# Performance work log

Hardware: AMD Instinct MI355X
Metric: run time of the kernel (lower is better)

## Reference

```python
import jax, jax.numpy as jnp
import numpy as np

D = 768
H = 12
HD = D // H
NQ = 100
KV = 257
SEQ = NQ + KV
BS = 32


def layer_norm(x, g, b):
    # torch LayerNorm computed in fp32 then cast back (LayerNorm subclass)
    xf = x.astype(jnp.float32)
    m = xf.mean(-1, keepdims=True)
    v = ((xf - m) ** 2).mean(-1, keepdims=True)
    return ((xf - m) / jnp.sqrt(v + 1e-5) * g + b).astype(x.dtype)


def setup_inputs() -> dict:
    key = jax.random.key(0)
    ks = jax.random.split(key, 8)
    s = 0.02
    return {
        "y": jax.random.normal(ks[0], (SEQ, BS, D), jnp.float32),
        "attn_mask": jax.random.bernoulli(ks[1], 0.3, (BS, NQ, KV)),
        "in_proj_w": jax.random.normal(ks[2], (3 * D, D), jnp.float32) * s,
        "in_proj_b": jnp.zeros((3 * D,), jnp.float32),
        "new_q_w": jax.random.normal(ks[3], (D, D), jnp.float32) * s,
        "new_q_b": jnp.zeros((D,), jnp.float32),
        "out_w": jax.random.normal(ks[4], (D, D), jnp.float32) * s,
        "out_b": jnp.zeros((D,), jnp.float32),
        "ln1_g": jnp.ones((D,), jnp.float32),
        "ln1_b": jnp.zeros((D,), jnp.float32),
        "ln2_g": jnp.ones((D,), jnp.float32),
        "ln2_b": jnp.zeros((D,), jnp.float32),
        "fc_w": jax.random.normal(ks[5], (4 * D, D), jnp.float32) * s,
        "fc_b": jnp.zeros((4 * D,), jnp.float32),
        "proj_w": jax.random.normal(ks[6], (D, 4 * D), jnp.float32) * s,
        "proj_b": jnp.zeros((D,), jnp.float32),
    }


def _attention(x, attn_mask, in_proj_w, in_proj_b, new_q_w, new_q_b, out_w, out_b):
    # x: [seq, bs, D] (already ln_1'd); attn_mask: [bs, nq, kv] bool
    seq, bs, d = x.shape
    nq = attn_mask.shape[1]
    scale = 1.0 / np.sqrt(HD)
    # k/v (and the clip queries) come from the detached non-query tokens
    xkv = jax.lax.stop_gradient(x[nq:])  # [kv, bs, D]
    qkv = xkv @ in_proj_w.T + in_proj_b
    q, k, v = jnp.split(qkv, 3, axis=-1)

    def heads(t):  # [S, bs, D] -> [bs, H, S, hd]
        return t.reshape(t.shape[0], bs, H, HD).transpose(1, 2, 0, 3)

    q = heads(q) * scale
    k = heads(k)
    v = heads(v)
    # regular (clip) attention over shared k/v
    clip_attn = jnp.einsum('bhld,bhmd->bhlm', q, k)
    clip_out = jnp.einsum('bhlm,bhmd->bhld', jax.nn.softmax(clip_attn, axis=-1), v)
    # mask-conditioned queries via new_q_proj (NOT detached)
    new_q = heads(x[:nq] @ new_q_w.T + new_q_b) * scale  # [bs, H, nq, hd]
    bias = jnp.where(attn_mask[:, None], -jnp.inf, 0.0).astype(q.dtype)  # [bs,1,nq,kv]
    mask_attn = jnp.einsum('bhqd,bhmd->bhqm', new_q, k) + bias
    mask_out = jnp.einsum('bhqm,bhmd->bhqd', jax.nn.softmax(mask_attn, axis=-1), v)

    def merge(t):  # [bs, H, S, hd] -> [S, bs, D]
        return t.transpose(2, 0, 1, 3).reshape(t.shape[2], bs, d)

    attn_out = jnp.concatenate([merge(mask_out), merge(clip_out)], axis=0)
    return attn_out @ out_w.T + out_b


def reference(y, attn_mask, in_proj_w, in_proj_b, new_q_w, new_q_b, out_w, out_b,
              ln1_g, ln1_b, ln2_g, ln2_b, fc_w, fc_b, proj_w, proj_b):
    x = layer_norm(y, ln1_g, ln1_b)
    y = y + _attention(x, attn_mask, in_proj_w, in_proj_b, new_q_w, new_q_b, out_w, out_b)
    h = layer_norm(y, ln2_g, ln2_b)
    h = h @ fc_w.T + fc_b
    h = h * jax.nn.sigmoid(1.702 * h)  # QuickGELU
    return y + (h @ proj_w.T + proj_b)
```

## Files before the change

### kernel.cpp

```cpp
#include <hip/hip_runtime.h>


typedef short bf16x8 __attribute__((ext_vector_type(8)));
typedef float f32x4 __attribute__((ext_vector_type(4)));
typedef unsigned short u16;
typedef unsigned long long u64;

__device__ __forceinline__ u16 f2b(float f) {
    unsigned u = __builtin_bit_cast(unsigned, f);
    u = (u + 0x7fffu + ((u >> 16) & 1u)) >> 16;
    return (u16)u;
}
__device__ __forceinline__ float b2f(u16 h) {
    unsigned u = ((unsigned)h) << 16;
    return __builtin_bit_cast(float, u);
}
__device__ __forceinline__ unsigned pack2(float a, float b) {
    return (unsigned)f2b(a) | ((unsigned)f2b(b) << 16);
}
__device__ __forceinline__ void g2l16(const void* g, void* l) {
    __builtin_amdgcn_global_load_lds(
        (__attribute__((address_space(1))) void*)g,
        (__attribute__((address_space(3))) void*)l, 16, 0, 0);
}

__global__ __launch_bounds__(256) void cvt5_kernel(
    const float* __restrict__ s0, const float* __restrict__ s1, const float* __restrict__ s2,
    const float* __restrict__ s3, const float* __restrict__ s4, u16* __restrict__ dst)
{
    int i = blockIdx.x * 256 + threadIdx.x;
    int stride = gridDim.x * 256;
    for (; i < 1916928; i += stride) {
        const float* src; int off;
        if (i < 442368)       { src = s0; off = i; }
        else if (i < 589824)  { src = s1; off = i - 442368; }
        else if (i < 737280)  { src = s2; off = i - 589824; }
        else if (i < 1327104) { src = s3; off = i - 737280; }
        else                  { src = s4; off = i - 1327104; }
        float4 v = ((const float4*)src)[off];
        ushort4 o;
        o.x = f2b(v.x); o.y = f2b(v.y); o.z = f2b(v.z); o.w = f2b(v.w);
        ((ushort4*)dst)[i] = o;
    }
}

__global__ __launch_bounds__(256) void mask_pack(const int* __restrict__ m, u64* __restrict__ o) {
    int row = blockIdx.x * 4 + (threadIdx.x >> 6);
    int lane = threadIdx.x & 63;
    if (row >= 3200) return;
    const int* r = m + (size_t)row * 257;
    u64 w0 = __ballot(r[lane] != 0);
    u64 w1 = __ballot(r[64 + lane] != 0);
    u64 w2 = __ballot(r[128 + lane] != 0);
    u64 w3 = __ballot(r[192 + lane] != 0);
    u64 w4 = __ballot(lane == 0 && r[256] != 0);
    if (lane == 0) {
        u64* p = o + (size_t)row * 5;
        p[0] = w0; p[1] = w1; p[2] = w2; p[3] = w3; p[4] = w4;
    }
}

__global__ __launch_bounds__(256) void ln_kernel(
    const float* __restrict__ in, const float* __restrict__ g, const float* __restrict__ be,
    u16* __restrict__ out, int nrows)
{
    int row = blockIdx.x * 4 + (threadIdx.x >> 6);
    int lane = threadIdx.x & 63;
    if (row >= nrows) return;
    const float* p = in + (size_t)row * 768;
    float4 a0 = *(const float4*)(p + lane * 4);
    float4 a1 = *(const float4*)(p + 256 + lane * 4);
    float4 a2 = *(const float4*)(p + 512 + lane * 4);
    float s = a0.x + a0.y + a0.z + a0.w + a1.x + a1.y + a1.z + a1.w + a2.x + a2.y + a2.z + a2.w;
    for (int o = 32; o; o >>= 1) s += __shfl_xor(s, o);
    float mean = s * (1.f / 768.f);
    float vs = 0.f;
#define SQA(t) { float dx; dx = t.x-mean; vs += dx*dx; dx = t.y-mean; vs += dx*dx; dx = t.z-mean; vs += dx*dx; dx = t.w-mean; vs += dx*dx; }
    SQA(a0) SQA(a1) SQA(a2)
#undef SQA
    for (int o = 32; o; o >>= 1) vs += __shfl_xor(vs, o);
    float rstd = rsqrtf(vs * (1.f / 768.f) + 1e-5f);
    u16* orow = out + (size_t)row * 768;
#pragma unroll
    for (int i = 0; i < 3; ++i) {
        int d = i * 256 + lane * 4;
        float4 av = (i == 0) ? a0 : ((i == 1) ? a1 : a2);
        float4 gv = *(const float4*)(g + d);
        float4 bv = *(const float4*)(be + d);
        ushort4 ov;
        ov.x = f2b((av.x - mean) * rstd * gv.x + bv.x);
        ov.y = f2b((av.y - mean) * rstd * gv.y + bv.y);
        ov.z = f2b((av.z - mean) * rstd * gv.z + bv.z);
        ov.w = f2b((av.w - mean) * rstd * gv.w + bv.w);
        *(ushort4*)(orow + d) = ov;
    }
}

template<int ACT, int OUTBF, int RES>
__global__ __launch_bounds__(256) void gemm_bt(
    const u16* __restrict__ A, const u16* __restrict__ B,
    const float* __restrict__ bias, const float* __restrict__ res,
    void* __restrict__ Cp, int M, int N, int K)
{
    __shared__ u16 Al[2][128 * 32];
    __shared__ u16 Bl[2][128 * 32];
    const int t = threadIdx.x;
    const int lane = t & 63, w = t >> 6;
    const int wr = w >> 1, wc = w & 1;
    const int m0 = blockIdx.x * 128, n0 = blockIdx.y * 128;
    const int fr = lane & 15, fg = lane >> 4;

    const int srow = lane >> 2;
    const int scol = (lane & 3) * 8;
    int ar0 = m0 + w * 32 + srow;      int ar1 = ar0 + 16;
    ar0 = ar0 < M ? ar0 : M - 1;       ar1 = ar1 < M ? ar1 : M - 1;
    int br0 = n0 + w * 32 + srow;      int br1 = br0 + 16;
    br0 = br0 < N ? br0 : N - 1;       br1 = br1 < N ? br1 : N - 1;
    const u16* a0p = A + (size_t)ar0 * K + scol;
    const u16* a1p = A + (size_t)ar1 * K + scol;
    const u16* b0p = B + (size_t)br0 * K + scol;
    const u16* b1p = B + (size_t)br1 * K + scol;
    const int lo0 = (w * 2 + 0) * 512, lo1 = (w * 2 + 1) * 512;

    const int nk = K >> 5;
    g2l16(a0p, &Al[0][lo0]);
    g2l16(a1p, &Al[0][lo1]);
    g2l16(b0p, &Bl[0][lo0]);
    g2l16(b1p, &Bl[0][lo1]);
    __syncthreads();

    f32x4 acc[4][4] = {};
#pragma unroll 2
    for (int ki = 0; ki < nk; ++ki) {
        const int cur = ki & 1;
        if (ki + 1 < nk) {
            const int k0 = (ki + 1) << 5;
            const int nxt = cur ^ 1;
            g2l16(a0p + k0, &Al[nxt][lo0]);
            g2l16(a1p + k0, &Al[nxt][lo1]);
            g2l16(b0p + k0, &Bl[nxt][lo0]);
            g2l16(b1p + k0, &Bl[nxt][lo1]);
        }
        bf16x8 af[4], bfr[4];
#pragma unroll
        for (int m = 0; m < 4; ++m) af[m] = *(const bf16x8*)&Al[cur][(wr * 64 + m * 16 + fr) * 32 + fg * 8];
#pragma unroll
        for (int n = 0; n < 4; ++n) bfr[n] = *(const bf16x8*)&Bl[cur][(wc * 64 + n * 16 + fr) * 32 + fg * 8];
#pragma unroll
        for (int m = 0; m < 4; ++m)
#pragma unroll
            for (int n = 0; n < 4; ++n)
                acc[m][n] = __builtin_amdgcn_mfma_f32_16x16x32_bf16(af[m], bfr[n], acc[m][n], 0, 0, 0);
        __syncthreads();
    }
#pragma unroll
    for (int m = 0; m < 4; ++m) {
#pragma unroll
        for (int n = 0; n < 4; ++n) {
            int col = n0 + wc * 64 + n * 16 + fr;
            float bv = bias[col];
#pragma unroll
            for (int r = 0; r < 4; ++r) {
                int row = m0 + wr * 64 + m * 16 + fg * 4 + r;
                if (row < M) {
                    float v = acc[m][n][r] + bv;
                    if (RES) v += res[(size_t)row * N + col];
                    if (ACT) v = v / (1.f + __expf(-1.702f * v));
                    if (OUTBF) ((u16*)Cp)[(size_t)row * N + col] = f2b(v);
                    else       ((float*)Cp)[(size_t)row * N + col] = v;
                }
            }
        }
    }
}

__global__ __launch_bounds__(256, 2) void attn_kernel(
    const u16* __restrict__ qkv,
    const u16* __restrict__ nq,
    const u64* __restrict__ mpk,
    u16* __restrict__ out)
{
    __shared__ u16 Kl[272 * 64];
    __shared__ u16 Vt[64 * 296];
    __shared__ u16 Pb[4][640];
    const int bid = blockIdx.x;
    const int b = bid / 12, h = bid % 12;
    const int t = threadIdx.x, lane = t & 63, wv = t >> 6;
    const int fr = lane & 15, fg = lane >> 4;

    for (int i = t; i < 2048; i += 256) {
        int d = i >> 5, c = 257 + (i & 31);
        if (c < 288) Vt[d * 296 + c] = 0;
    }
    {
        const int r8 = t >> 3, c8 = (t & 7) * 8;
        const u16* kb = qkv + 768 + h * 64 + c8;
        const u16* vb = qkv + 1536 + h * 64 + c8;
#pragma unroll 1
        for (int p = 0; p < 9; ++p) {
            int m = r8 + p * 32;
            if (m <= 256) {
                size_t go = (size_t)(m * 32 + b) * 2304;
                bf16x8 kv = *(const bf16x8*)(kb + go);
                int byte = m * 128 + c8 * 2;
                *(bf16x8*)((char*)Kl + (byte ^ ((m & 7) << 4))) = kv;
                bf16x8 vv = *(const bf16x8*)(vb + go);
#pragma unroll
                for (int j = 0; j < 8; ++j)
                    Vt[(c8 + j) * 296 + m] = (u16)vv[j];
            }
        }
    }
    __syncthreads();

    const int swzK = (fr & 7) << 4;
    char* pb = (char*)&Pb[wv][0];
    const char* KlB = (const char*)Kl;
    const char* VtB = (const char*)Vt;

    auto fetch = [&](int ti, bf16x8& q0v, bf16x8& q1v, u64* mw, bool& im) {
        int q = ti * 16 + fr;
        int qc = q < 357 ? q : 356;
        im = qc < 100;
        const u16* qp = im ? (nq + (size_t)(qc * 32 + b) * 768 + h * 64)
                           : (qkv + (size_t)((qc - 100) * 32 + b) * 2304 + h * 64);
        q0v = *(const bf16x8*)(qp + fg * 8);
        q1v = *(const bf16x8*)(qp + 32 + fg * 8);
        if (im) {
            const u64* mp = mpk + (size_t)(b * 100 + qc) * 5;
            mw[0] = mp[0]; mw[1] = mp[1]; mw[2] = mp[2]; mw[3] = mp[3]; mw[4] = mp[4];
        } else {
            mw[0] = mw[1] = mw[2] = mw[3] = mw[4] = 0;
        }
    };

    bf16x8 qf0, qf1, qn0, qn1;
    u64 mwc[5], mwn[5];
    bool imc, imn;
    fetch(wv, qf0, qf1, mwc, imc);

#pragma unroll 1
    for (int ti = wv; ti < 23; ti += 4) {
        f32x4 sc[17];
#pragma unroll
        for (int kt = 0; kt < 17; ++kt) {
            int rb = (kt * 16 + fr) * 128;
            bf16x8 ka0 = *(const bf16x8*)(KlB + ((rb + fg * 16) ^ swzK));
            bf16x8 ka1 = *(const bf16x8*)(KlB + ((rb + 64 + fg * 16) ^ swzK));
            f32x4 a = {0.f, 0.f, 0.f, 0.f};
            a = __builtin_amdgcn_mfma_f32_16x16x32_bf16(ka0, qf0, a, 0, 0, 0);
            a = __builtin_amdgcn_mfma_f32_16x16x32_bf16(ka1, qf1, a, 0, 0, 0);
            sc[kt] = a;
        }
        if (ti + 4 < 23) fetch(ti + 4, qn0, qn1, mwn, imn);
        float mx = -INFINITY;
#pragma unroll
        for (int kt = 0; kt < 17; ++kt) {
            u64 mw = (kt >> 2) == 0 ? mwc[0] : (kt >> 2) == 1 ? mwc[1] : (kt >> 2) == 2 ? mwc[2]
                   : (kt >> 2) == 3 ? mwc[3] : mwc[4];
#pragma unroll
            for (int r = 0; r < 4; ++r) {
                int key = kt * 16 + fg * 4 + r;
                bool bad = (key > 256) || (imc && ((mw >> (key & 63)) & 1ull));
                float s = bad ? -INFINITY : sc[kt][r];
                sc[kt][r] = s;
                mx = fmaxf(mx, s);
            }
        }
        mx = fmaxf(mx, __shfl_xor(mx, 16));
        mx = fmaxf(mx, __shfl_xor(mx, 32));
        float l = 0.f;
        unsigned pk[17][2];
#pragma unroll
        for (int kt = 0; kt < 17; ++kt) {
            float p0 = __expf((sc[kt][0] - mx) * 0.125f);
            float p1 = __expf((sc[kt][1] - mx) * 0.125f);
            float p2 = __expf((sc[kt][2] - mx) * 0.125f);
            float p3 = __expf((sc[kt][3] - mx) * 0.125f);
            l += (p0 + p1) + (p2 + p3);
            pk[kt][0] = pack2(p0, p1);
            pk[kt][1] = pack2(p2, p3);
        }
        l += __shfl_xor(l, 16);
        l += __shfl_xor(l, 32);
        f32x4 oc[4] = {};
#pragma unroll
        for (int c = 0; c < 9; ++c) {
            uint2 w0; w0.x = pk[2 * c][0]; w0.y = pk[2 * c][1];
            *(uint2*)(pb + fr * 80 + fg * 8) = w0;
            uint2 w1;
            if (c < 8) { w1.x = pk[2 * c + 1][0]; w1.y = pk[2 * c + 1][1]; }
            else       { w1.x = 0; w1.y = 0; }
            *(uint2*)(pb + fr * 80 + 32 + fg * 8) = w1;
            bf16x8 pf = *(const bf16x8*)(pb + fr * 80 + fg * 16);
#pragma unroll
            for (int dt = 0; dt < 4; ++dt) {
                bf16x8 vf = *(const bf16x8*)(VtB + (dt * 16 + fr) * 592 + c * 64 + fg * 16);
                oc[dt] = __builtin_amdgcn_mfma_f32_16x16x32_bf16(vf, pf, oc[dt], 0, 0, 0);
            }
        }
        int q = ti * 16 + fr;
        if (q < 357) {
            float rl = 1.f / l;
            u16* op = out + (size_t)(q * 32 + b) * 768 + h * 64 + fg * 4;
#pragma unroll
            for (int dt = 0; dt < 4; ++dt) {
                ushort4 ov;
                ov.x = f2b(oc[dt][0] * rl); ov.y = f2b(oc[dt][1] * rl);
                ov.z = f2b(oc[dt][2] * rl); ov.w = f2b(oc[dt][3] * rl);
                *(ushort4*)(op + dt * 16) = ov;
            }
        }
        if (ti + 4 < 23) {
            qf0 = qn0; qf1 = qn1; imc = imn;
            mwc[0] = mwn[0]; mwc[1] = mwn[1]; mwc[2] = mwn[2]; mwc[3] = mwn[3]; mwc[4] = mwn[4];
        }
    }
}

extern "C" void kernel_launch(void* const* d_in, const int* in_sizes, int n_in,
                              void* d_out, int out_size, void* d_ws, size_t ws_size,
                              hipStream_t stream)
{
    const float* y   = (const float*)d_in[0];
    const int*   msk = (const int*)  d_in[1];
    const float* ipw = (const float*)d_in[2];
    const float* ipb = (const float*)d_in[3];
    const float* nqw = (const float*)d_in[4];
    const float* nqb = (const float*)d_in[5];
    const float* ow  = (const float*)d_in[6];
    const float* ob  = (const float*)d_in[7];
    const float* l1g = (const float*)d_in[8];
    const float* l1b = (const float*)d_in[9];
    const float* l2g = (const float*)d_in[10];
    const float* l2b = (const float*)d_in[11];
    const float* fcw = (const float*)d_in[12];
    const float* fcb = (const float*)d_in[13];
    const float* pjw = (const float*)d_in[14];
    const float* pjb = (const float*)d_in[15];

    char* ws = (char*)d_ws;
    u16* x_b   = (u16*)(ws + 0);
    u16* qkv_b = (u16*)(ws + 17547264);
    u16* nq_b  = (u16*)(ws + 55443456);
    u16* ao_b  = (u16*)(ws + 60358656);
    u16* h1_b  = (u16*)(ws + 0);
    u16* h_b   = (u16*)(ws + 77905920);
    u64* mpk_b = (u64*)(ws + 77905920);
    u16* w_ip  = (u16*)(ws + 95453184);
    float* out = (float*)d_out;

    cvt5_kernel<<<2048, 256, 0, stream>>>(ipw, nqw, ow, fcw, pjw, w_ip);
    mask_pack<<<800, 256, 0, stream>>>(msk, mpk_b);

    u16* w_nq  = w_ip + 1769472;
    u16* w_out = w_nq + 589824;
    u16* w_fc  = w_out + 589824;
    u16* w_pj  = w_fc + 2359296;

    ln_kernel<<<2856, 256, 0, stream>>>(y, l1g, l1b, x_b, 11424);
    gemm_bt<0, 1, 0><<<dim3(65, 18), 256, 0, stream>>>(x_b + (size_t)3200 * 768, w_ip, ipb, nullptr, qkv_b, 8224, 2304, 768);
    gemm_bt<0, 1, 0><<<dim3(25, 6), 256, 0, stream>>>(x_b, w_nq, nqb, nullptr, nq_b, 3200, 768, 768);
    attn_kernel<<<384, 256, 0, stream>>>(qkv_b, nq_b, mpk_b, ao_b);
    gemm_bt<0, 0, 1><<<dim3(90, 6), 256, 0, stream>>>(ao_b, w_out, ob, y, out, 11424, 768, 768);
    ln_kernel<<<2856, 256, 0, stream>>>(out, l2g, l2b, h_b, 11424);
    gemm_bt<1, 1, 0><<<dim3(90, 24), 256, 0, stream>>>(h_b, w_fc, fcb, nullptr, h1_b, 11424, 3072, 768);
    gemm_bt<0, 0, 1><<<dim3(90, 6), 256, 0, stream>>>(h1_b, w_pj, pjb, out, out, 11424, 768, 3072);
}
```

Baseline: 470.6 us.

## Add 256x256 eight-wave GEMM with interleaved staging and XCD remap

Introduces a 256x256-tile GEMM kernel with 512 threads, double-buffered global-to-LDS loads interleaved with MFMA quarter-blocks, s_setprio around the compute phases, swizzled LDS, and an XCD-aware block remap. It replaces the 128-tile GEMM for the QKV, output, FC and projection matmuls. The goal is higher data reuse per tile and better overlap of loads with MFMA. The trade-off is fewer workgroups, e.g. 135 blocks for the N=768 GEMMs, which may leave CUs idle, and clamped rows at the M boundary add some redundant loads.

```diff
diff --git a/kernel.cpp b/kernel.cpp
--- a/kernel.cpp
+++ b/kernel.cpp
@@ -23,6 +23,14 @@
         (__attribute__((address_space(1))) void*)g,
         (__attribute__((address_space(3))) void*)l, 16, 0, 0);
 }
+#define MFMA16(a, b, c) __builtin_amdgcn_mfma_f32_16x16x32_bf16((a), (b), (c), 0, 0, 0)
+#define BAR() __builtin_amdgcn_s_barrier()
+#define SP1() __builtin_amdgcn_s_setprio(1)
+#define SP0() __builtin_amdgcn_s_setprio(0)
+#define LGK0() do { asm volatile("s_waitcnt lgkmcnt(0)" ::: "memory"); \
+                    __builtin_amdgcn_sched_barrier(0); } while (0)
+#define VM4()  do { asm volatile("s_waitcnt vmcnt(4)" ::: "memory"); \
+                    __builtin_amdgcn_sched_barrier(0); } while (0)
 
 __global__ __launch_bounds__(256) void cvt5_kernel(
     const float* __restrict__ s0, const float* __restrict__ s1, const float* __restrict__ s2,
@@ -150,7 +158,7 @@
         for (int m = 0; m < 4; ++m)
 #pragma unroll
             for (int n = 0; n < 4; ++n)
-                acc[m][n] = __builtin_amdgcn_mfma_f32_16x16x32_bf16(af[m], bfr[n], acc[m][n], 0, 0, 0);
+                acc[m][n] = MFMA16(af[m], bfr[n], acc[m][n]);
         __syncthreads();
     }
 #pragma unroll
@@ -164,6 +172,142 @@
                 int row = m0 + wr * 64 + m * 16 + fg * 4 + r;
                 if (row < M) {
                     float v = acc[m][n][r] + bv;
+                    if (RES) v += res[(size_t)row * N + col];
+                    if (ACT) v = v / (1.f + __expf(-1.702f * v));
+                    if (OUTBF) ((u16*)Cp)[(size_t)row * N + col] = f2b(v);
+                    else       ((float*)Cp)[(size_t)row * N + col] = v;
+                }
+            }
+        }
+    }
+}
+
+template<int ACT, int OUTBF, int RES>
+__global__ __launch_bounds__(512) void gemm256(
+    const u16* __restrict__ A, const u16* __restrict__ B,
+    const float* __restrict__ bias, const float* __restrict__ res,
+    void* __restrict__ Cp, int M, int N, int K)
+{
+    __shared__ u16 lds[65536];
+    const int t = threadIdx.x, lane = t & 63, w = t >> 6;
+    const int wr = w >> 2, wc = w & 3;
+    const int fr = lane & 15, fg = lane >> 4;
+
+    const int nwg = gridDim.x * gridDim.y;
+    int orig = blockIdx.x + gridDim.x * blockIdx.y;
+    {
+        int q = nwg >> 3, r = nwg & 7;
+        int xcd = orig & 7, idx = orig >> 3;
+        orig = (xcd < r ? xcd * (q + 1) : r * (q + 1) + (xcd - r) * q) + idx;
+    }
+    const int m0 = (orig % gridDim.x) * 256;
+    const int n0 = (orig / gridDim.x) * 256;
+
+    const int nkt = K >> 6;
+    char* ldsB = (char*)lds;
+    const int jrow = lane >> 3;
+    const int swz = ((lane & 7) ^ jrow) * 8;
+
+    auto stageA = [&](int b, int h, int kt) {
+        int r0 = m0 + h * 128 + w * 16 + jrow;
+        int r1 = r0 + 8;
+        r0 = r0 < M ? r0 : M - 1;
+        r1 = r1 < M ? r1 : M - 1;
+        char* lb = ldsB + b * 65536 + h * 16384 + w * 2048;
+        g2l16(A + (size_t)r0 * K + kt * 64 + swz, lb);
+        g2l16(A + (size_t)r1 * K + kt * 64 + swz, lb + 1024);
+    };
+    auto stageB = [&](int b, int h, int kt) {
+        int r0 = n0 + h * 128 + w * 16 + jrow;
+        char* lb = ldsB + b * 65536 + 32768 + h * 16384 + w * 2048;
+        g2l16(B + (size_t)r0 * K + kt * 64 + swz, lb);
+        g2l16(B + (size_t)(r0 + 8) * K + kt * 64 + swz, lb + 1024);
+    };
+    auto ldA = [&](int b, int mi, int kh) -> bf16x8 {
+        int lr = mi * 16 + fr;
+        int slot = (fg + 4 * kh) ^ (lr & 7);
+        return *(const bf16x8*)(ldsB + b * 65536 + wr * 16384 + lr * 128 + slot * 16);
+    };
+    auto ldB = [&](int b, int ni, int kh) -> bf16x8 {
+        int lr = (wc & 1) * 64 + ni * 16 + fr;
+        int slot = (fg + 4 * kh) ^ (lr & 7);
+        return *(const bf16x8*)(ldsB + b * 65536 + 32768 + (wc >> 1) * 16384 + lr * 128 + slot * 16);
+    };
+
+    f32x4 acc[8][4] = {};
+
+    stageB(0, 0, 0); stageB(0, 1, 0); stageA(0, 0, 0); stageA(0, 1, 0);
+    stageB(1, 0, 1); stageB(1, 1, 1);
+    VM4(); BAR();
+
+    auto halfiter = [&](int bc, int ba, int ta, int bb, int tb) {
+        bf16x8 aa[4][2], bn0[2][2], bn1[2][2];
+#pragma unroll
+        for (int mi = 0; mi < 4; ++mi) { aa[mi][0] = ldA(bc, mi, 0); aa[mi][1] = ldA(bc, mi, 1); }
+#pragma unroll
+        for (int ni = 0; ni < 2; ++ni) { bn0[ni][0] = ldB(bc, ni, 0); bn0[ni][1] = ldB(bc, ni, 1); }
+        if (ta < nkt) stageA(ba, 0, ta);
+        BAR(); LGK0(); SP1();
+#pragma unroll
+        for (int mi = 0; mi < 4; ++mi)
+#pragma unroll
+            for (int ni = 0; ni < 2; ++ni) {
+                acc[mi][ni] = MFMA16(aa[mi][0], bn0[ni][0], acc[mi][ni]);
+                acc[mi][ni] = MFMA16(aa[mi][1], bn0[ni][1], acc[mi][ni]);
+            }
+        SP0(); BAR();
+#pragma unroll
+        for (int ni = 0; ni < 2; ++ni) { bn1[ni][0] = ldB(bc, 2 + ni, 0); bn1[ni][1] = ldB(bc, 2 + ni, 1); }
+        if (ta < nkt) stageA(ba, 1, ta);
+        BAR(); LGK0(); SP1();
+#pragma unroll
+        for (int mi = 0; mi < 4; ++mi)
+#pragma unroll
+            for (int ni = 0; ni < 2; ++ni) {
+                acc[mi][2 + ni] = MFMA16(aa[mi][0], bn1[ni][0], acc[mi][2 + ni]);
+                acc[mi][2 + ni] = MFMA16(aa[mi][1], bn1[ni][1], acc[mi][2 + ni]);
+            }
+        SP0(); BAR();
+#pragma unroll
+        for (int mi = 0; mi < 4; ++mi) { aa[mi][0] = ldA(bc, 4 + mi, 0); aa[mi][1] = ldA(bc, 4 + mi, 1); }
+        if (tb < nkt) stageB(bb, 0, tb);
+        BAR(); LGK0(); SP1();
+#pragma unroll
+        for (int mi = 0; mi < 4; ++mi)
+#pragma unroll
+            for (int ni = 0; ni < 2; ++ni) {
+                acc[4 + mi][ni] = MFMA16(aa[mi][0], bn0[ni][0], acc[4 + mi][ni]);
+                acc[4 + mi][ni] = MFMA16(aa[mi][1], bn0[ni][1], acc[4 + mi][ni]);
+            }
+        SP0(); BAR();
+        if (tb < nkt) stageB(bb, 1, tb);
+        BAR(); SP1();
+#pragma unroll
+        for (int mi = 0; mi < 4; ++mi)
+#pragma unroll
+            for (int ni = 0; ni < 2; ++ni) {
+                acc[4 + mi][2 + ni] = MFMA16(aa[mi][0], bn1[ni][0], acc[4 + mi][2 + ni]);
+                acc[4 + mi][2 + ni] = MFMA16(aa[mi][1], bn1[ni][1], acc[4 + mi][2 + ni]);
+            }
+        SP0(); VM4(); BAR();
+    };
+
+    for (int i = 0; i < nkt; i += 2) {
+        halfiter(0, 1, i + 1, 0, i + 2);
+        halfiter(1, 0, i + 2, 1, i + 3);
+    }
+
+#pragma unroll
+    for (int mi = 0; mi < 8; ++mi) {
+#pragma unroll
+        for (int ni = 0; ni < 4; ++ni) {
+            int col = n0 + wc * 64 + ni * 16 + fr;
+            float bv = bias[col];
+#pragma unroll
+            for (int rr = 0; rr < 4; ++rr) {
+                int row = m0 + wr * 128 + mi * 16 + fg * 4 + rr;
+                if (row < M) {
+                    float v = acc[mi][ni][rr] + bv;
                     if (RES) v += res[(size_t)row * N + col];
                     if (ACT) v = v / (1.f + __expf(-1.702f * v));
                     if (OUTBF) ((u16*)Cp)[(size_t)row * N + col] = f2b(v);
@@ -248,8 +392,8 @@
             bf16x8 ka0 = *(const bf16x8*)(KlB + ((rb + fg * 16) ^ swzK));
             bf16x8 ka1 = *(const bf16x8*)(KlB + ((rb + 64 + fg * 16) ^ swzK));
             f32x4 a = {0.f, 0.f, 0.f, 0.f};
-            a = __builtin_amdgcn_mfma_f32_16x16x32_bf16(ka0, qf0, a, 0, 0, 0);
-            a = __builtin_amdgcn_mfma_f32_16x16x32_bf16(ka1, qf1, a, 0, 0, 0);
+            a = MFMA16(ka0, qf0, a);
+            a = MFMA16(ka1, qf1, a);
             sc[kt] = a;
         }
         if (ti + 4 < 23) fetch(ti + 4, qn0, qn1, mwn, imn);
@@ -296,7 +440,7 @@
 #pragma unroll
             for (int dt = 0; dt < 4; ++dt) {
                 bf16x8 vf = *(const bf16x8*)(VtB + (dt * 16 + fr) * 592 + c * 64 + fg * 16);
-                oc[dt] = __builtin_amdgcn_mfma_f32_16x16x32_bf16(vf, pf, oc[dt], 0, 0, 0);
+                oc[dt] = MFMA16(vf, pf, oc[dt]);
             }
         }
         int q = ti * 16 + fr;
@@ -359,11 +503,11 @@
     u16* w_pj  = w_fc + 2359296;
 
     ln_kernel<<<2856, 256, 0, stream>>>(y, l1g, l1b, x_b, 11424);
-    gemm_bt<0, 1, 0><<<dim3(65, 18), 256, 0, stream>>>(x_b + (size_t)3200 * 768, w_ip, ipb, nullptr, qkv_b, 8224, 2304, 768);
+    gemm256<0, 1, 0><<<dim3(33, 9), 512, 0, stream>>>(x_b + (size_t)3200 * 768, w_ip, ipb, nullptr, qkv_b, 8224, 2304, 768);
     gemm_bt<0, 1, 0><<<dim3(25, 6), 256, 0, stream>>>(x_b, w_nq, nqb, nullptr, nq_b, 3200, 768, 768);
     attn_kernel<<<384, 256, 0, stream>>>(qkv_b, nq_b, mpk_b, ao_b);
-    gemm_bt<0, 0, 1><<<dim3(90, 6), 256, 0, stream>>>(ao_b, w_out, ob, y, out, 11424, 768, 768);
+    gemm256<0, 0, 1><<<dim3(45, 3), 512, 0, stream>>>(ao_b, w_out, ob, y, out, 11424, 768, 768);
     ln_kernel<<<2856, 256, 0, stream>>>(out, l2g, l2b, h_b, 11424);
-    gemm_bt<1, 1, 0><<<dim3(90, 24), 256, 0, stream>>>(h_b, w_fc, fcb, nullptr, h1_b, 11424, 3072, 768);
-    gemm_bt<0, 0, 1><<<dim3(90, 6), 256, 0, stream>>>(h1_b, w_pj, pjb, out, out, 11424, 768, 3072);
-}
+    gemm256<1, 1, 0><<<dim3(45, 12), 512, 0, stream>>>(h_b, w_fc, fcb, nullptr, h1_b, 11424, 3072, 768);
+    gemm256<0, 0, 1><<<dim3(45, 3), 512, 0, stream>>>(h1_b, w_pj, pjb, out, out, 11424, 768, 3072);
+}
```

After: 562.5 us. 19.5% more time.

## Triple-buffer GEMM LDS staging with explicit vmcnt waits and single barrier

Applied to the files above, without the earlier changes.

Moves the GEMM main loop from double to triple buffering of the A/B LDS tiles, issuing loads two K-steps ahead. It replaces __syncthreads with explicit s_waitcnt vmcnt(4)/vmcnt(0) plus a raw s_barrier, so later loads can stay in flight while the current tile is consumed. The intent is to hide global-to-LDS latency better. In exchange it uses more LDS per block (48KB), which may reduce occupancy, and it relies on hand-counted vmcnt for correctness.

```diff
diff --git a/kernel.cpp b/kernel.cpp
--- a/kernel.cpp
+++ b/kernel.cpp
@@ -23,6 +23,12 @@
         (__attribute__((address_space(1))) void*)g,
         (__attribute__((address_space(3))) void*)l, 16, 0, 0);
 }
+#define MFMA16(a, b, c) __builtin_amdgcn_mfma_f32_16x16x32_bf16((a), (b), (c), 0, 0, 0)
+#define BAR() __builtin_amdgcn_s_barrier()
+#define VM4() do { asm volatile("s_waitcnt vmcnt(4)" ::: "memory"); \
+                   __builtin_amdgcn_sched_barrier(0); } while (0)
+#define VM0() do { asm volatile("s_waitcnt vmcnt(0)" ::: "memory"); \
+                   __builtin_amdgcn_sched_barrier(0); } while (0)
 
 __global__ __launch_bounds__(256) void cvt5_kernel(
     const float* __restrict__ s0, const float* __restrict__ s1, const float* __restrict__ s2,
@@ -102,8 +108,8 @@
     const float* __restrict__ bias, const float* __restrict__ res,
     void* __restrict__ Cp, int M, int N, int K)
 {
-    __shared__ u16 Al[2][128 * 32];
-    __shared__ u16 Bl[2][128 * 32];
+    __shared__ u16 Al[3][128 * 32];
+    __shared__ u16 Bl[3][128 * 32];
     const int t = threadIdx.x;
     const int lane = t & 63, w = t >> 6;
     const int wr = w >> 1, wc = w & 1;
@@ -123,35 +129,37 @@
     const int lo0 = (w * 2 + 0) * 512, lo1 = (w * 2 + 1) * 512;
 
     const int nk = K >> 5;
-    g2l16(a0p, &Al[0][lo0]);
-    g2l16(a1p, &Al[0][lo1]);
-    g2l16(b0p, &Bl[0][lo0]);
-    g2l16(b1p, &Bl[0][lo1]);
-    __syncthreads();
+    auto stage = [&](int ki, int bsel) {
+        const int k0 = ki << 5;
+        g2l16(a0p + k0, &Al[bsel][lo0]);
+        g2l16(a1p + k0, &Al[bsel][lo1]);
+        g2l16(b0p + k0, &Bl[bsel][lo0]);
+        g2l16(b1p + k0, &Bl[bsel][lo1]);
+    };
+    stage(0, 0);
+    stage(1, 1);
+    VM4();
+    BAR();
 
     f32x4 acc[4][4] = {};
-#pragma unroll 2
+#pragma unroll 3
     for (int ki = 0; ki < nk; ++ki) {
-        const int cur = ki & 1;
+        const int cur = ki % 3;
+        if (ki + 2 < nk) stage(ki + 2, (ki + 2) % 3);
+        bf16x8 af[4], bfr[4];
+#pragma unroll
+        for (int m = 0; m < 4; ++m) af[m] = *(const bf16x8*)&Al[cur][(wr * 64 + m * 16 + fr) * 32 + fg * 8];
+#pragma unroll
+        for (int n = 0; n < 4; ++n) bfr[n] = *(const bf16x8*)&Bl[cur][(wc * 64 + n * 16 + fr) * 32 + fg * 8];
+#pragma unroll
+        for (int m = 0; m < 4; ++m)
+#pragma unroll
+            for (int n = 0; n < 4; ++n)
+                acc[m][n] = MFMA16(af[m], bfr[n], acc[m][n]);
         if (ki + 1 < nk) {
-            const int k0 = (ki + 1) << 5;
-            const int nxt = cur ^ 1;
-            g2l16(a0p + k0, &Al[nxt][lo0]);
-            g2l16(a1p + k0, &Al[nxt][lo1]);
-            g2l16(b0p + k0, &Bl[nxt][lo0]);
-            g2l16(b1p + k0, &Bl[nxt][lo1]);
-        }
-        bf16x8 af[4], bfr[4];
-#pragma unroll
-        for (int m = 0; m < 4; ++m) af[m] = *(const bf16x8*)&Al[cur][(wr * 64 + m * 16 + fr) * 32 + fg * 8];
-#pragma unroll
-        for (int n = 0; n < 4; ++n) bfr[n] = *(const bf16x8*)&Bl[cur][(wc * 64 + n * 16 + fr) * 32 + fg * 8];
-#pragma unroll
-        for (int m = 0; m < 4; ++m)
-#pragma unroll
-            for (int n = 0; n < 4; ++n)
-                acc[m][n] = __builtin_amdgcn_mfma_f32_16x16x32_bf16(af[m], bfr[n], acc[m][n], 0, 0, 0);
-        __syncthreads();
+            if (ki + 2 < nk) { VM4(); } else { VM0(); }
+            BAR();
+        }
     }
 #pragma unroll
     for (int m = 0; m < 4; ++m) {
@@ -248,8 +256,8 @@
             bf16x8 ka0 = *(const bf16x8*)(KlB + ((rb + fg * 16) ^ swzK));
             bf16x8 ka1 = *(const bf16x8*)(KlB + ((rb + 64 + fg * 16) ^ swzK));
             f32x4 a = {0.f, 0.f, 0.f, 0.f};
-            a = __builtin_amdgcn_mfma_f32_16x16x32_bf16(ka0, qf0, a, 0, 0, 0);
-            a = __builtin_amdgcn_mfma_f32_16x16x32_bf16(ka1, qf1, a, 0, 0, 0);
+            a = MFMA16(ka0, qf0, a);
+            a = MFMA16(ka1, qf1, a);
             sc[kt] = a;
         }
         if (ti + 4 < 23) fetch(ti + 4, qn0, qn1, mwn, imn);
@@ -296,7 +304,7 @@
 #pragma unroll
             for (int dt = 0; dt < 4; ++dt) {
                 bf16x8 vf = *(const bf16x8*)(VtB + (dt * 16 + fr) * 592 + c * 64 + fg * 16);
-                oc[dt] = __builtin_amdgcn_mfma_f32_16x16x32_bf16(vf, pf, oc[dt], 0, 0, 0);
+                oc[dt] = MFMA16(vf, pf, oc[dt]);
             }
         }
         int q = ti * 16 + fr;
```

After: 490.5 us. 4.2% more time.
